# Optimization experiments

Hardware: AMD Instinct MI355X
Metric: run time of the kernel (lower is better)

The kernel has to match this reference:

```python
import jax, jax.numpy as jnp
import numpy as np

N, K, P, C, H, E, Q, G = 50000, 8, 512, 64, 128, 1600000, 500000, 64

def _gelu(x):
    return jax.nn.gelu(x, approximate=False)  # torch F.gelu default = exact erf

def _mlp(x, Wi, bi, Wh, bh, Wo, bo, Wp=None, bp=None):
    # MLP: lin_in -> gelu -> hid -> (proj skip if in>hidden) -> skip+gelu -> lin_out
    skip = x if Wp is None else x @ Wp.T + bp
    h = _gelu(x @ Wi.T + bi)
    h = h @ Wh.T + bh
    return (skip + _gelu(h)) @ Wo.T + bo

def _sage(x, src, dst, Wl, bl, Wr, n):
    # PyG SAGEConv: mean-aggregate source features at dst, then lin_l(agg)+lin_r(x)
    s = jax.ops.segment_sum(x[src], dst, num_segments=n)
    cnt = jax.ops.segment_sum(jnp.ones((src.shape[0], 1), x.dtype), dst, num_segments=n)
    agg = s / jnp.maximum(cnt, 1.0)
    return agg @ Wl.T + bl + x @ Wr.T

def setup_inputs():
    key = jax.random.key(0)
    ks = iter(jax.random.split(key, 64))
    def lin(o, i):
        return (jax.random.normal(next(ks), (o, i), jnp.float32) / np.sqrt(i)).astype(jnp.float32)
    def bias(o):
        return jnp.zeros((o,), jnp.float32)
    inp = {}
    inp["x"] = jax.random.normal(next(ks), (N, K, P), jnp.float32)
    inp["batch"] = jnp.sort(jax.random.randint(next(ks), (N,), 0, G))
    inp["edge_index"] = jax.random.randint(next(ks), (2, E), 0, N)
    inp["src_idx"] = jax.random.randint(next(ks), (Q,), 0, N)
    inp["dst_idx"] = jax.random.randint(next(ks), (Q,), 0, N)
    # Embedder.mlp : MLP(P, P, H) with proj (P > H)
    inp.update(em_in_W=lin(H, P), em_in_b=bias(H), em_hid_W=lin(H, H), em_hid_b=bias(H),
               em_out_W=lin(P, H), em_out_b=bias(P), em_proj_W=lin(H, P), em_proj_b=bias(H))
    # Embedder.rho : MLP(P, C, H) with proj
    inp.update(rho_in_W=lin(H, P), rho_in_b=bias(H), rho_hid_W=lin(H, H), rho_hid_b=bias(H),
               rho_out_W=lin(C, H), rho_out_b=bias(C), rho_proj_W=lin(H, P), rho_proj_b=bias(H))
    for i in (1, 2, 3):
        inp[f"c{i}_ll_W"] = lin(C, C); inp[f"c{i}_ll_b"] = bias(C); inp[f"c{i}_lr_W"] = lin(C, C)
    # head MLP(3C, 2C, 2C) with proj (3C > 2C)
    inp.update(h1_in_W=lin(H, 3 * C), h1_in_b=bias(H), h1_hid_W=lin(H, H), h1_hid_b=bias(H),
               h1_out_W=lin(2 * C, H), h1_out_b=bias(2 * C), h1_proj_W=lin(H, 3 * C), h1_proj_b=bias(H))
    # head MLP(2C, 1, 2C), no proj
    inp.update(h2_in_W=lin(H, 2 * C), h2_in_b=bias(H), h2_hid_W=lin(H, H), h2_hid_b=bias(H),
               h2_out_W=lin(1, H), h2_out_b=bias(1))
    return inp

def reference(x, batch, edge_index, src_idx, dst_idx,
              em_in_W, em_in_b, em_hid_W, em_hid_b, em_out_W, em_out_b, em_proj_W, em_proj_b,
              rho_in_W, rho_in_b, rho_hid_W, rho_hid_b, rho_out_W, rho_out_b, rho_proj_W, rho_proj_b,
              c1_ll_W, c1_ll_b, c1_lr_W, c2_ll_W, c2_ll_b, c2_lr_W, c3_ll_W, c3_ll_b, c3_lr_W,
              h1_in_W, h1_in_b, h1_hid_W, h1_hid_b, h1_out_W, h1_out_b, h1_proj_W, h1_proj_b,
              h2_in_W, h2_in_b, h2_hid_W, h2_hid_b, h2_out_W, h2_out_b):
    n = x.shape[0]
    # Embedder: per-point MLP, gelu, sum over point-set dim, then rho (dropout = eval identity)
    h = _gelu(_mlp(x, em_in_W, em_in_b, em_hid_W, em_hid_b, em_out_W, em_out_b, em_proj_W, em_proj_b))
    z = _mlp(h.sum(-2), rho_in_W, rho_in_b, rho_hid_W, rho_hid_b, rho_out_W, rho_out_b, rho_proj_W, rho_proj_b)
    src, dst = edge_index[0], edge_index[1]
    z = z + _gelu(_sage(z, src, dst, c1_ll_W, c1_ll_b, c1_lr_W, n))
    z = z + _gelu(_sage(z, src, dst, c2_ll_W, c2_ll_b, c2_lr_W, n))
    z = z + _gelu(_sage(z, src, dst, c3_ll_W, c3_ll_b, c3_lr_W, n))
    node_embeddings = z
    # global_max_pool keyed by batch id, broadcast back via gather
    graph_emb = jax.ops.segment_max(z, batch, num_segments=G)
    ge = graph_emb[batch[src_idx]]  # == graph_emb[batch][src_idx]
    se, de = z[src_idx], z[dst_idx]
    xy = jnp.concatenate([se, de, ge], axis=-1)
    yx = jnp.concatenate([de, se, ge], axis=-1)
    def head(q):
        t = jax.nn.relu(_mlp(q, h1_in_W, h1_in_b, h1_hid_W, h1_hid_b, h1_out_W, h1_out_b, h1_proj_W, h1_proj_b))
        return _mlp(t, h2_in_W, h2_in_b, h2_hid_W, h2_hid_b, h2_out_W, h2_out_b)
    return (node_embeddings, (head(xy), head(yx)), xy)
```

## Files before the change

### kernel.cpp

```cpp
#include <hip/hip_runtime.h>

typedef unsigned short US;
typedef unsigned int   UI;
typedef short  short8 __attribute__((ext_vector_type(8)));
typedef US     u16x8  __attribute__((ext_vector_type(8)));
typedef float  f32x4  __attribute__((ext_vector_type(4)));

#define DEVI __device__ __forceinline__

DEVI float bf2f(US u){ UI i = ((UI)u) << 16; float f; __builtin_memcpy(&f, &i, 4); return f; }
DEVI US f2bf(float x){ UI i; __builtin_memcpy(&i, &x, 4); UI r = (i + 0x7FFFu + ((i >> 16) & 1u)) >> 16; return (US)r; }
DEVI float gelu_f(float x){
    float x2 = x * x;
    float u  = x * fmaf(x2, 0.0713548193f, 1.5957691216f);
    float e  = __expf(-u);
    return x / (1.0f + e);
}
DEVI UI encf(float f){ UI u; __builtin_memcpy(&u, &f, 4); return (u & 0x80000000u) ? ~u : (u | 0x80000000u); }
DEVI float decf(UI u){ UI b = (u & 0x80000000u) ? (u ^ 0x80000000u) : ~u; float f; __builtin_memcpy(&f, &b, 4); return f; }
DEVI int swz(int r, int c, int ld){ int i = r * ld + c; return i ^ ((r & 7) << 3); }

DEVI UI pkbf(float a, float b){ UI u; asm("v_cvt_pk_bf16_f32 %0, %1, %2" : "=v"(u) : "v"(a), "v"(b)); return u; }
DEVI void st4(US* T, int row, int col, float v0, float v1, float v2, float v3){
    uint2 p; p.x = pkbf(v0, v1); p.y = pkbf(v2, v3);
    *(uint2*)&T[swz(row, col, 256)] = p;
}
DEVI void ld4(const US* T, int row, int col, float& v0, float& v1, float& v2, float& v3){
    uint2 q = *(const uint2*)&T[swz(row, col, 256)];
    v0 = bf2f((US)(q.x & 0xffff)); v1 = bf2f((US)(q.x >> 16));
    v2 = bf2f((US)(q.y & 0xffff)); v3 = bf2f((US)(q.y >> 16));
}

enum : int { O_EmW1 = 0, O_EmWh = 131072, O_EmWo = 147456, O_RhoW1 = 212992,
             O_RhoWh = 344064, O_RhoWo = 360448, O_Cat1 = 368640, O_Cat2 = 376832,
             O_Cat3 = 385024, O_H1W1 = 393216, O_H1Wh = 442368, O_H1Wo = 458752,
             O_H2W1 = 475136, O_H2Wh = 491520, W_TOTAL = 507904 };

template<int NT, int NKC, int NTHR, bool SWAP = false>
DEVI void stageWD(const US* __restrict__ Wg, int Kw, const US* __restrict__ A, int lda,
                  int ab0, int ab1, int ab2, int arow0, US* Wb, int tid, f32x4 (&acc)[NT])
{
    const int lane = tid & 63;
    const int wc = (tid >> 6) & 1;
    constexpr int SLAB = NT * 32 * 64;
    #pragma unroll
    for (int n = 0; n < NT; ++n) acc[n] = (f32x4){0.f, 0.f, 0.f, 0.f};
    constexpr int J = (NT * 256) / NTHR;
    u16x8 wreg[J];
    #pragma unroll
    for (int j = 0; j < J; ++j) {
        const int c = tid + NTHR * j;
        wreg[j] = *(const u16x8*)(Wg + (size_t)(c >> 3) * Kw + (c & 7) * 8);
    }
    #pragma unroll
    for (int j = 0; j < J; ++j) {
        const int c = tid + NTHR * j;
        *(u16x8*)&Wb[swz(c >> 3, (c & 7) * 8, 64)] = wreg[j];
    }
    #pragma unroll
    for (int kc = 0; kc < NKC; ++kc) {
        __syncthreads();
        if (kc + 1 < NKC) {
            #pragma unroll
            for (int j = 0; j < J; ++j) {
                const int c = tid + NTHR * j;
                wreg[j] = *(const u16x8*)(Wg + (size_t)(c >> 3) * Kw + (kc + 1) * 64 + (c & 7) * 8);
            }
        }
        const int ab = (kc == 0) ? ab0 : ((kc == 1) ? ab1 : ab2);
        const int bufr = (kc & 1) * SLAB;
        #pragma unroll
        for (int sub = 0; sub < 2; ++sub) {
            const int kk = sub * 32 + ((lane >> 4) << 3);
            short8 a = *(const short8*)&A[swz(arow0 + (lane & 15), ab + kk, lda)];
            #pragma unroll
            for (int n = 0; n < NT; ++n) {
                short8 b = *(const short8*)&Wb[bufr + swz(wc * (NT * 16) + n * 16 + (lane & 15), kk, 64)];
                if (SWAP) acc[n] = __builtin_amdgcn_mfma_f32_16x16x32_bf16(b, a, acc[n], 0, 0, 0);
                else      acc[n] = __builtin_amdgcn_mfma_f32_16x16x32_bf16(a, b, acc[n], 0, 0, 0);
            }
        }
        if (kc + 1 < NKC) {
            const int bufw = ((kc + 1) & 1) * SLAB;
            #pragma unroll
            for (int j = 0; j < J; ++j) {
                const int c = tid + NTHR * j;
                *(u16x8*)&Wb[bufw + swz(c >> 3, (c & 7) * 8, 64)] = wreg[j];
            }
        }
    }
    __syncthreads();
}

__global__ __launch_bounds__(1024, 4)
void embed_fused(const float* __restrict__ x, const US* __restrict__ WB,
                 const float* __restrict__ b_in, const float* __restrict__ b_proj,
                 const float* __restrict__ b_hid, const float* __restrict__ b_out,
                 US* __restrict__ Ss)
{
    __shared__ __align__(16) US T1[128 * 256];
    __shared__ __align__(16) US Wb[2 * 16384];
    __shared__ __align__(16) US As[128 * 64];
    const int tid = threadIdx.x, lane = tid & 63, w = tid >> 6;
    const int wr = w >> 1, wc = w & 1;
    const int grow0 = blockIdx.x * 128;
    const int row0 = wr * 16 + ((lane >> 4) << 2);

    {
        f32x4 acc[8];
        #pragma unroll
        for (int n = 0; n < 8; ++n) acc[n] = (f32x4){0.f, 0.f, 0.f, 0.f};
        const float* xr = x + (size_t)(grow0 + (tid >> 3)) * 512 + (tid & 7) * 8;
        float4 a0, a1;
        u16x8 wreg[2];
        auto loadA = [&](int kc) { a0 = *(const float4*)(xr + kc * 64); a1 = *(const float4*)(xr + kc * 64 + 4); };
        auto loadW = [&](int kc) {
            #pragma unroll
            for (int j = 0; j < 2; ++j) {
                const int c = tid + 1024 * j;
                wreg[j] = *(const u16x8*)(WB + O_EmW1 + (size_t)(c >> 3) * 512 + kc * 64 + (c & 7) * 8);
            }
        };
        loadA(0); loadW(0);
        for (int kc = 0; kc < 8; ++kc) {
            __syncthreads();
            {
                u16x8 v;
                v[0] = f2bf(a0.x); v[1] = f2bf(a0.y); v[2] = f2bf(a0.z); v[3] = f2bf(a0.w);
                v[4] = f2bf(a1.x); v[5] = f2bf(a1.y); v[6] = f2bf(a1.z); v[7] = f2bf(a1.w);
                *(u16x8*)&As[swz(tid >> 3, (tid & 7) * 8, 64)] = v;
                #pragma unroll
                for (int j = 0; j < 2; ++j) {
                    const int c = tid + 1024 * j;
                    *(u16x8*)&Wb[swz(c >> 3, (c & 7) * 8, 64)] = wreg[j];
                }
            }
            __syncthreads();
            if (kc < 7) { loadA(kc + 1); loadW(kc + 1); }
            #pragma unroll
            for (int sub = 0; sub < 2; ++sub) {
                const int kk = sub * 32 + ((lane >> 4) << 3);
                short8 a = *(const short8*)&As[swz(wr * 16 + (lane & 15), kk, 64)];
                #pragma unroll
                for (int n = 0; n < 8; ++n) {
                    short8 b = *(const short8*)&Wb[swz(wc * 128 + n * 16 + (lane & 15), kk, 64)];
                    acc[n] = __builtin_amdgcn_mfma_f32_16x16x32_bf16(a, b, acc[n], 0, 0, 0);
                }
            }
        }
        __syncthreads();
        #pragma unroll
        for (int n = 0; n < 8; ++n) {
            const int col = wc * 128 + n * 16 + (lane & 15);
            const float bv = (col < 128) ? b_in[col] : b_proj[col - 128];
            #pragma unroll
            for (int r = 0; r < 4; ++r) {
                float v = acc[n][r] + bv;
                if (col < 128) v = gelu_f(v);
                T1[swz(row0 + r, col, 256)] = f2bf(v);
            }
        }
    }
    {
        f32x4 acc[4];
        stageWD<4, 2, 1024>(WB + O_EmWh, 128, T1, 256, 0, 64, 0, wr * 16, Wb, tid, acc);
        #pragma unroll
        for (int n = 0; n < 4; ++n) {
            const int col = wc * 64 + n * 16 + (lane & 15);
            const float bv = b_hid[col];
            #pragma unroll
            for (int r = 0; r < 4; ++r) {
                const float sv = bf2f(T1[swz(row0 + r, 128 + col, 256)]);
                T1[swz(row0 + r, col, 256)] = f2bf(gelu_f(acc[n][r] + bv) + sv);
            }
        }
    }
    for (int p2 = 0; p2 < 2; ++p2) {
        f32x4 acc[8];
        stageWD<8, 2, 1024>(WB + O_EmWo + (size_t)(p2 * 256) * 128, 128, T1, 256, 0, 64, 0, wr * 16, Wb, tid, acc);
        #pragma unroll
        for (int n = 0; n < 8; ++n) {
            const int col = wc * 128 + n * 16 + (lane & 15);
            const float bv = b_out[p2 * 256 + col];
            float s = 0.f;
            #pragma unroll
            for (int r = 0; r < 4; ++r) s += gelu_f(acc[n][r] + bv);
            s += __shfl_xor(s, 16);
            if (((lane >> 4) & 1) == 0) {
                const int node = (grow0 >> 3) + wr * 2 + (lane >> 5);
                Ss[(size_t)node * 512 + p2 * 256 + col] = f2bf(s);
            }
        }
    }
}

__global__ __launch_bounds__(512, 2)
void rho_fused(const US* __restrict__ Ss, const US* __restrict__ WB,
               const float* __restrict__ b_in, const float* __restrict__ b_proj,
               const float* __restrict__ b_hid, const float* __restrict__ b_out,
               US* __restrict__ zo, int N)
{
    __shared__ __align__(16) US T1[64 * 256];
    __shared__ __align__(16) US Wb[256 * 64];
    __shared__ __align__(16) US As[64 * 64];
    const int tid = threadIdx.x, lane = tid & 63, w = tid >> 6;
    const int wr = w >> 1, wc = w & 1;
    const int grow0 = blockIdx.x * 64;
    const int row0 = wr * 16 + ((lane >> 4) << 2);

    {
        f32x4 acc[8];
        #pragma unroll
        for (int n = 0; n < 8; ++n) acc[n] = (f32x4){0.f, 0.f, 0.f, 0.f};
        int arow = grow0 + (tid >> 3); if (arow >= N) arow = N - 1;
        const US* srow = Ss + (size_t)arow * 512 + (tid & 7) * 8;
        u16x8 areg, wreg[4];
        auto loadA = [&](int kc) { areg = *(const u16x8*)(srow + kc * 64); };
        auto loadW = [&](int kc) {
            #pragma unroll
            for (int j = 0; j < 4; ++j) {
                const int c = tid + 512 * j;
                wreg[j] = *(const u16x8*)(WB + O_RhoW1 + (size_t)(c >> 3) * 512 + kc * 64 + (c & 7) * 8);
            }
        };
        loadA(0); loadW(0);
        for (int kc = 0; kc < 8; ++kc) {
            __syncthreads();
            *(u16x8*)&As[swz(tid >> 3, (tid & 7) * 8, 64)] = areg;
            #pragma unroll
            for (int j = 0; j < 4; ++j) {
                const int c = tid + 512 * j;
                *(u16x8*)&Wb[swz(c >> 3, (c & 7) * 8, 64)] = wreg[j];
            }
            __syncthreads();
            if (kc < 7) { loadA(kc + 1); loadW(kc + 1); }
            #pragma unroll
            for (int sub = 0; sub < 2; ++sub) {
                const int kk = sub * 32 + ((lane >> 4) << 3);
                short8 a = *(const short8*)&As[swz(wr * 16 + (lane & 15), kk, 64)];
                #pragma unroll
                for (int n = 0; n < 8; ++n) {
                    short8 b = *(const short8*)&Wb[swz(wc * 128 + n * 16 + (lane & 15), kk, 64)];
                    acc[n] = __builtin_amdgcn_mfma_f32_16x16x32_bf16(a, b, acc[n], 0, 0, 0);
                }
            }
        }
        __syncthreads();
        #pragma unroll
        for (int n = 0; n < 8; ++n) {
            const int col = wc * 128 + n * 16 + (lane & 15);
            const float bv = (col < 128) ? b_in[col] : b_proj[col - 128];
            #pragma unroll
            for (int r = 0; r < 4; ++r) {
                float v = acc[n][r] + bv;
                if (col < 128) v = gelu_f(v);
                T1[swz(row0 + r, col, 256)] = f2bf(v);
            }
        }
    }
    {
        f32x4 acc[4];
        stageWD<4, 2, 512>(WB + O_RhoWh, 128, T1, 256, 0, 64, 0, wr * 16, Wb, tid, acc);
        #pragma unroll
        for (int n = 0; n < 4; ++n) {
            const int col = wc * 64 + n * 16 + (lane & 15);
            const float bv = b_hid[col];
            #pragma unroll
            for (int r = 0; r < 4; ++r) {
                const float sv = bf2f(T1[swz(row0 + r, 128 + col, 256)]);
                T1[swz(row0 + r, col, 256)] = f2bf(gelu_f(acc[n][r] + bv) + sv);
            }
        }
    }
    {
        f32x4 acc[2];
        stageWD<2, 2, 512>(WB + O_RhoWo, 128, T1, 256, 0, 64, 0, wr * 16, Wb, tid, acc);
        #pragma unroll
        for (int n = 0; n < 2; ++n) {
            const int col = wc * 32 + n * 16 + (lane & 15);
            const float bv = b_out[col];
            #pragma unroll
            for (int r = 0; r < 4; ++r) {
                const int node = grow0 + row0 + r;
                if (node < N) zo[(size_t)node * 64 + col] = f2bf(acc[n][r] + bv);
            }
        }
    }
}

__global__ __launch_bounds__(1024, 4)
void head_fused(const int* __restrict__ srcq, const int* __restrict__ dstq,
                const int* __restrict__ batch, const US* __restrict__ z,
                const US* __restrict__ geb, const US* __restrict__ WB,
                const float* __restrict__ b1_in, const float* __restrict__ b1_proj,
                const float* __restrict__ b1_hid, const float* __restrict__ b1_out,
                const float* __restrict__ b2_in, const float* __restrict__ b2_hid,
                const float* __restrict__ w2_out, const float* __restrict__ b2_out,
                float* __restrict__ outH, float* __restrict__ outXY, int Q)
{
    __shared__ __align__(16) US A0[64 * 192];
    __shared__ __align__(16) US T1[128 * 256];
    __shared__ __align__(16) US Wb[2 * 16384];
    __shared__ float wout_s[128];
    const int tid = threadIdx.x, lane = tid & 63, w = tid >> 6;
    const int wr = w >> 1, wc = w & 1;
    const int q0 = blockIdx.x * 64;
    const int s1a = (wr < 4) ? 0 : 64;
    const int s1b = (wr < 4) ? 64 : 0;
    const int arowS1 = (wr & 3) * 16;
    const int rowS1 = (wr >> 2) * 64 + arowS1 + (lane & 15);
    const int rowT  = wr * 16 + (lane & 15);
    {
        if (tid < 512) {
            const int r = tid >> 3, h = tid & 7;
            const int q = q0 + r;
            const int qc = (q < Q) ? q : (Q - 1);
            const int s = srcq[qc], d = dstq[qc];
            const int g = batch[s];
            *(u16x8*)&A0[swz(r, h * 8, 192)]       = *(const u16x8*)(z + (size_t)s * 64 + h * 8);
            *(u16x8*)&A0[swz(r, 64 + h * 8, 192)]  = *(const u16x8*)(z + (size_t)d * 64 + h * 8);
            *(u16x8*)&A0[swz(r, 128 + h * 8, 192)] = *(const u16x8*)(geb + (size_t)g * 64 + h * 8);
        }
        if (tid < 128) wout_s[tid] = w2_out[tid];
    }
    __syncthreads();
    {
        #pragma unroll
        for (int jj = 0; jj < 3; ++jj) {
            const int f = tid + 1024 * jj;
            const int row = f / 48;
            const int c4 = (f - row * 48) * 4;
            if (q0 + row < Q) {
                const US* p = &A0[swz(row, c4, 192)];
                float4 o;
                o.x = bf2f(p[0]); o.y = bf2f(p[1]); o.z = bf2f(p[2]); o.w = bf2f(p[3]);
                *(float4*)&outXY[(size_t)(q0 + row) * 192 + c4] = o;
            }
        }
    }
    {
        f32x4 acc8[8];
        stageWD<8, 3, 1024, true>(WB + O_H1W1, 192, A0, 192, s1a, s1b, 128, arowS1, Wb, tid, acc8);
        #pragma unroll
        for (int n = 0; n < 8; ++n) {
            const int col = wc * 128 + n * 16 + ((lane >> 4) << 2);
            float4 bv = (col < 128) ? *(const float4*)&b1_in[col]
                                    : *(const float4*)&b1_proj[col - 128];
            float v0 = acc8[n][0] + bv.x, v1 = acc8[n][1] + bv.y;
            float v2 = acc8[n][2] + bv.z, v3 = acc8[n][3] + bv.w;
            if (col < 128) { v0 = gelu_f(v0); v1 = gelu_f(v1); v2 = gelu_f(v2); v3 = gelu_f(v3); }
            st4(T1, rowS1, col, v0, v1, v2, v3);
        }
    }
    f32x4 acc[4];
    stageWD<4, 2, 1024, true>(WB + O_H1Wh, 128, T1, 256, 0, 64, 0, wr * 16, Wb, tid, acc);
    #pragma unroll
    for (int n = 0; n < 4; ++n) {
        const int col = wc * 64 + n * 16 + ((lane >> 4) << 2);
        float4 bv = *(const float4*)&b1_hid[col];
        float s0, s1, s2, s3;
        ld4(T1, rowT, 128 + col, s0, s1, s2, s3);
        st4(T1, rowT, col,
            gelu_f(acc[0 + n][0] * 0.f + acc[n][0] + bv.x) + s0,
            gelu_f(acc[n][1] + bv.y) + s1,
            gelu_f(acc[n][2] + bv.z) + s2,
            gelu_f(acc[n][3] + bv.w) + s3);
    }
    stageWD<4, 2, 1024, true>(WB + O_H1Wo, 128, T1, 256, 0, 64, 0, wr * 16, Wb, tid, acc);
    #pragma unroll
    for (int n = 0; n < 4; ++n) {
        const int col = wc * 64 + n * 16 + ((lane >> 4) << 2);
        float4 bv = *(const float4*)&b1_out[col];
        st4(T1, rowT, 128 + col,
            fmaxf(acc[n][0] + bv.x, 0.f), fmaxf(acc[n][1] + bv.y, 0.f),
            fmaxf(acc[n][2] + bv.z, 0.f), fmaxf(acc[n][3] + bv.w, 0.f));
    }
    stageWD<4, 2, 1024, true>(WB + O_H2W1, 128, T1, 256, 128, 192, 0, wr * 16, Wb, tid, acc);
    #pragma unroll
    for (int n = 0; n < 4; ++n) {
        const int col = wc * 64 + n * 16 + ((lane >> 4) << 2);
        float4 bv = *(const float4*)&b2_in[col];
        st4(T1, rowT, col,
            gelu_f(acc[n][0] + bv.x), gelu_f(acc[n][1] + bv.y),
            gelu_f(acc[n][2] + bv.z), gelu_f(acc[n][3] + bv.w));
    }
    stageWD<4, 2, 1024, true>(WB + O_H2Wh, 128, T1, 256, 0, 64, 0, wr * 16, Wb, tid, acc);
    #pragma unroll
    for (int n = 0; n < 4; ++n) {
        const int col = wc * 64 + n * 16 + ((lane >> 4) << 2);
        float4 bv = *(const float4*)&b2_hid[col];
        float t0, t1, t2, t3;
        ld4(T1, rowT, 128 + col, t0, t1, t2, t3);
        st4(T1, rowT, col,
            gelu_f(acc[n][0] + bv.x) + t0, gelu_f(acc[n][1] + bv.y) + t1,
            gelu_f(acc[n][2] + bv.z) + t2, gelu_f(acc[n][3] + bv.w) + t3);
    }
    __syncthreads();
    {
        const int r = tid >> 3, h = tid & 7;
        float a = 0.f;
        u16x8 v0 = *(const u16x8*)&T1[swz(r, h * 16, 256)];
        u16x8 v1 = *(const u16x8*)&T1[swz(r, h * 16 + 8, 256)];
        #pragma unroll
        for (int e = 0; e < 8; ++e) {
            a += bf2f(v0[e]) * wout_s[h * 16 + e];
            a += bf2f(v1[e]) * wout_s[h * 16 + 8 + e];
        }
        a += __shfl_xor(a, 4);
        a += __shfl_xor(a, 2);
        a += __shfl_xor(a, 1);
        const int q = q0 + (r & 63);
        if ((lane & 7) == 0 && q < Q) outH[(size_t)(r >> 6) * Q + q] = a + b2_out[0];
    }
}

__global__ __launch_bounds__(256, 2)
void sage_gemm(const US* __restrict__ zin, const US* __restrict__ agg,
               const US* __restrict__ Wc, const float* __restrict__ bias,
               US* __restrict__ zout, int N)
{
    __shared__ __align__(16) US As[128 * 128];
    __shared__ __align__(16) US Ws[64 * 128];
    const int tid = threadIdx.x, lane = tid & 63, w = tid >> 6;
    const int grow0 = blockIdx.x * 128;
    {
        const int r = tid >> 1, h = tid & 1;
        int row = grow0 + r; if (row >= N) row = N - 1;
        const US* src = h ? (zin + (size_t)row * 64) : (agg + (size_t)row * 64);
        #pragma unroll
        for (int j = 0; j < 8; ++j)
            *(u16x8*)&As[swz(r, h * 64 + 8 * j, 128)] = *(const u16x8*)(src + 8 * j);
    }
    #pragma unroll
    for (int j = 0; j < 4; ++j) {
        const int c = tid + 256 * j;
        *(u16x8*)&Ws[swz(c >> 4, (c & 15) * 8, 128)] =
            *(const u16x8*)(Wc + (size_t)(c >> 4) * 128 + (c & 15) * 8);
    }
    __syncthreads();
    const int rbw = w * 32;
    f32x4 acc[2][4];
    #pragma unroll
    for (int m = 0; m < 2; ++m)
        #pragma unroll
        for (int n = 0; n < 4; ++n) acc[m][n] = (f32x4){0.f, 0.f, 0.f, 0.f};
    #pragma unroll
    for (int kc = 0; kc < 2; ++kc)
        #pragma unroll
        for (int sub = 0; sub < 2; ++sub) {
            const int kk = kc * 64 + sub * 32 + ((lane >> 4) << 3);
            short8 a[2], b[4];
            #pragma unroll
            for (int m = 0; m < 2; ++m) a[m] = *(const short8*)&As[swz(rbw + m * 16 + (lane & 15), kk, 128)];
            #pragma unroll
            for (int n = 0; n < 4; ++n) b[n] = *(const short8*)&Ws[swz(n * 16 + (lane & 15), kk, 128)];
            #pragma unroll
            for (int m = 0; m < 2; ++m)
                #pragma unroll
                for (int n = 0; n < 4; ++n)
                    acc[m][n] = __builtin_amdgcn_mfma_f32_16x16x32_bf16(a[m], b[n], acc[m][n], 0, 0, 0);
        }
    #pragma unroll
    for (int m = 0; m < 2; ++m) {
        const int row0 = rbw + m * 16 + ((lane >> 4) << 2);
        #pragma unroll
        for (int n = 0; n < 4; ++n) {
            const int col = n * 16 + (lane & 15);
            const float bv = bias[col];
            #pragma unroll
            for (int r = 0; r < 4; ++r) {
                const int node = grow0 + row0 + r;
                if (node < N) {
                    const float v = gelu_f(acc[m][n][r] + bv) + bf2f(zin[(size_t)node * 64 + col]);
                    zout[(size_t)node * 64 + col] = f2bf(v);
                }
            }
        }
    }
}

struct WSeg { const float* src; int dst; int n; int rl; int ldd; };
struct WPrm { WSeg s[20]; };

__global__ void prep_w(WPrm p, US* __restrict__ wb)
{
    WSeg sg = p.s[blockIdx.x];
    for (int i = threadIdx.x; i < sg.n; i += 256) {
        const int idx = sg.dst + (i / sg.rl) * sg.ldd + (i % sg.rl);
        wb[idx] = f2bf(sg.src[i]);
    }
}

__global__ void count_k(const int* __restrict__ dst, int* __restrict__ cnt, int E)
{
    int e = blockIdx.x * 256 + threadIdx.x;
    if (e < E) atomicAdd(&cnt[dst[e]], 1);
}

__global__ void scan_csr(const int* __restrict__ cnt, int n, int* __restrict__ indp, int* __restrict__ curs)
{
    __shared__ int wsum[16];
    __shared__ int carry_s;
    const int tid = threadIdx.x, lane = tid & 63, w = tid >> 6;
    if (tid == 0) carry_s = 0;
    __syncthreads();
    for (int base = 0; base < n; base += 1024) {
        const int i = base + tid;
        const int v = (i < n) ? cnt[i] : 0;
        int s = v;
        #pragma unroll
        for (int o = 1; o < 64; o <<= 1) { int t = __shfl_up(s, o); if (lane >= o) s += t; }
        if (lane == 63) wsum[w] = s;
        __syncthreads();
        if (w == 0 && lane < 16) {
            int ws2 = wsum[lane];
            #pragma unroll
            for (int o = 1; o < 16; o <<= 1) { int t = __shfl_up(ws2, o); if (lane >= o) ws2 += t; }
            wsum[lane] = ws2;
        }
        __syncthreads();
        const int carry = carry_s;
        const int woff  = (w == 0) ? 0 : wsum[w - 1];
        if (i < n) { const int excl = carry + woff + s - v; indp[i] = excl; curs[i] = excl; }
        __syncthreads();
        if (tid == 0) carry_s = carry + wsum[15];
        __syncthreads();
    }
    if (threadIdx.x == 0) indp[n] = carry_s;
}

__global__ void fill_k(const int* __restrict__ src, const int* __restrict__ dst,
                       int* __restrict__ curs, int* __restrict__ esrc, int E)
{
    int e = blockIdx.x * 256 + threadIdx.x;
    if (e < E) { int p = atomicAdd(&curs[dst[e]], 1); esrc[p] = src[e]; }
}

__global__ void sage_agg(const US* __restrict__ z, const int* __restrict__ indp,
                         const int* __restrict__ esrc, US* __restrict__ agg, int n)
{
    const int w = blockIdx.x * 4 + (threadIdx.x >> 6);
    const int lane = threadIdx.x & 63;
    if (w >= n) return;
    const int beg = indp[w], end = indp[w + 1];
    float acc = 0.f;
    int j = beg;
    for (; j + 4 <= end; j += 4) {
        const int s0 = esrc[j], s1 = esrc[j + 1], s2 = esrc[j + 2], s3 = esrc[j + 3];
        const float v0 = bf2f(z[(size_t)s0 * 64 + lane]);
        const float v1 = bf2f(z[(size_t)s1 * 64 + lane]);
        const float v2 = bf2f(z[(size_t)s2 * 64 + lane]);
        const float v3 = bf2f(z[(size_t)s3 * 64 + lane]);
        acc += (v0 + v1) + (v2 + v3);
    }
    for (; j < end; ++j) acc += bf2f(z[(size_t)esrc[j] * 64 + lane]);
    const float d = (float)(end - beg);
    agg[(size_t)w * 64 + lane] = f2bf(acc / fmaxf(d, 1.0f));
}

__global__ void segmax_k(const US* __restrict__ z, const int* __restrict__ batch,
                         UI* __restrict__ enc, int n, int per)
{
    const int w = blockIdx.x * 4 + (threadIdx.x >> 6);
    const int lane = threadIdx.x & 63;
    const int start = w * per;
    if (start >= n) return;
    const int end = (start + per < n) ? start + per : n;
    int g = batch[start];
    float m = -3.0e38f;
    for (int i = start; i < end; ++i) {
        const int b = batch[i];
        if (b != g) { atomicMax(&enc[(size_t)g * 64 + lane], encf(m)); g = b; m = -3.0e38f; }
        m = fmaxf(m, bf2f(z[(size_t)i * 64 + lane]));
    }
    atomicMax(&enc[(size_t)g * 64 + lane], encf(m));
}

__global__ void decode_ge(const UI* __restrict__ enc, US* __restrict__ geb)
{
    const int i = blockIdx.x * 256 + threadIdx.x;
    if (i < 4096) geb[i] = f2bf(decf(enc[i]));
}

__global__ void copy_bf2f(const US* __restrict__ z, float* __restrict__ o, long n)
{
    long i = (long)blockIdx.x * blockDim.x + threadIdx.x;
    const long stride = (long)gridDim.x * blockDim.x;
    for (; i < n; i += stride) o[i] = bf2f(z[i]);
}

extern "C" void kernel_launch(void* const* d_in, const int* in_sizes, int n_in,
                              void* d_out, int out_size, void* d_ws, size_t ws_size,
                              hipStream_t stream)
{
    (void)in_sizes; (void)n_in; (void)out_size; (void)ws_size;

    const float* x      = (const float*)d_in[0];
    const int*   batch  = (const int*)d_in[1];
    const int*   eidx   = (const int*)d_in[2];
    const int*   srcq   = (const int*)d_in[3];
    const int*   dstq   = (const int*)d_in[4];
    const float* em_in_b   = (const float*)d_in[6];
    const float* em_hid_b  = (const float*)d_in[8];
    const float* em_out_b  = (const float*)d_in[10];
    const float* em_proj_b = (const float*)d_in[12];
    const float* rho_in_b  = (const float*)d_in[14];
    const float* rho_hid_b = (const float*)d_in[16];
    const float* rho_out_b = (const float*)d_in[18];
    const float* rho_proj_b= (const float*)d_in[20];
    const float* c_ll_W[3] = {(const float*)d_in[21], (const float*)d_in[24], (const float*)d_in[27]};
    const float* c_ll_b[3] = {(const float*)d_in[22], (const float*)d_in[25], (const float*)d_in[28]};
    const float* c_lr_W[3] = {(const float*)d_in[23], (const float*)d_in[26], (const float*)d_in[29]};
    const float* h1_in_b   = (const float*)d_in[31];
    const float* h1_hid_b  = (const float*)d_in[33];
    const float* h1_out_b  = (const float*)d_in[35];
    const float* h1_proj_b = (const float*)d_in[37];
    const float* h2_in_b   = (const float*)d_in[39];
    const float* h2_hid_b  = (const float*)d_in[41];
    const float* h2_out_W  = (const float*)d_in[42];
    const float* h2_out_b  = (const float*)d_in[43];

    const int N = 50000, E = 1600000, Q = 500000;
    float* out = (float*)d_out;

    char* wsb = (char*)d_ws;
    size_t off = 0;
    auto ALLOC = [&](size_t bytes) -> char* {
        char* p = wsb + off; off = (off + bytes + 255) & ~(size_t)255; return p;
    };
    US*  WB   = (US*)ALLOC((size_t)W_TOTAL * 2);
    US*  Ss   = (US*)ALLOC((size_t)N * 512 * 2);
    US*  z0   = (US*)ALLOC((size_t)N * 64 * 2);
    US*  z1   = (US*)ALLOC((size_t)N * 64 * 2);
    US*  aggB = (US*)ALLOC((size_t)N * 64 * 2);
    int* cnt  = (int*)ALLOC((size_t)N * 4);
    int* indp = (int*)ALLOC((size_t)(N + 1) * 4);
    int* curs = (int*)ALLOC((size_t)N * 4);
    int* esrc = (int*)ALLOC((size_t)E * 4);
    UI*  enc  = (UI*)ALLOC(4096 * 4);
    US*  geb  = (US*)ALLOC(4096 * 2);

    const int catOff[3] = {O_Cat1, O_Cat2, O_Cat3};

    WPrm pw; int si = 0;
    auto SEG = [&](const float* s, int o, int n, int rl, int ldd) {
        pw.s[si].src = s; pw.s[si].dst = o; pw.s[si].n = n; pw.s[si].rl = rl; pw.s[si].ldd = ldd; ++si;
    };
    SEG((const float*)d_in[5],  O_EmW1,          65536, 65536, 65536);
    SEG((const float*)d_in[11], O_EmW1 + 65536,  65536, 65536, 65536);
    SEG((const float*)d_in[7],  O_EmWh,          16384, 16384, 16384);
    SEG((const float*)d_in[9],  O_EmWo,          65536, 65536, 65536);
    SEG((const float*)d_in[13], O_RhoW1,         65536, 65536, 65536);
    SEG((const float*)d_in[19], O_RhoW1 + 65536, 65536, 65536, 65536);
    SEG((const float*)d_in[15], O_RhoWh,         16384, 16384, 16384);
    SEG((const float*)d_in[17], O_RhoWo,          8192,  8192,  8192);
    for (int i = 0; i < 3; ++i) {
        SEG(c_ll_W[i], catOff[i],      4096, 64, 128);
        SEG(c_lr_W[i], catOff[i] + 64, 4096, 64, 128);
    }
    SEG((const float*)d_in[30], O_H1W1,          24576, 24576, 24576);
    SEG((const float*)d_in[36], O_H1W1 + 24576,  24576, 24576, 24576);
    SEG((const float*)d_in[32], O_H1Wh,          16384, 16384, 16384);
    SEG((const float*)d_in[34], O_H1Wo,          16384, 16384, 16384);
    SEG((const float*)d_in[38], O_H2W1,          16384, 16384, 16384);
    SEG((const float*)d_in[40], O_H2Wh,          16384, 16384, 16384);
    prep_w<<<dim3(20), dim3(256), 0, stream>>>(pw, WB);

    hipMemsetAsync(cnt, 0, (size_t)N * 4, stream);
    count_k<<<dim3((E + 255) / 256), dim3(256), 0, stream>>>(eidx + E, cnt, E);
    scan_csr<<<dim3(1), dim3(1024), 0, stream>>>(cnt, N, indp, curs);
    fill_k<<<dim3((E + 255) / 256), dim3(256), 0, stream>>>(eidx, eidx + E, curs, esrc, E);

    embed_fused<<<dim3(3125), dim3(1024), 0, stream>>>(x, WB, em_in_b, em_proj_b, em_hid_b, em_out_b, Ss);
    rho_fused<<<dim3((N + 63) / 64), dim3(512), 0, stream>>>(Ss, WB, rho_in_b, rho_proj_b, rho_hid_b, rho_out_b, z0, N);

    US* zin = z0; US* zout = z1;
    for (int ci = 0; ci < 3; ++ci) {
        sage_agg<<<dim3((N + 3) / 4), dim3(256), 0, stream>>>(zin, indp, esrc, aggB, N);
        sage_gemm<<<dim3((N + 127) / 128), dim3(256), 0, stream>>>(zin, aggB, WB + catOff[ci], c_ll_b[ci], zout, N);
        US* t = zin; zin = zout; zout = t;
    }
    US* zf = zin;

    hipMemsetAsync(enc, 0, 4096 * 4, stream);
    segmax_k<<<dim3((N + 511) / 512), dim3(256), 0, stream>>>(zf, batch, enc, N, 128);
    decode_ge<<<dim3(16), dim3(256), 0, stream>>>(enc, geb);

    copy_bf2f<<<dim3(2048), dim3(256), 0, stream>>>(zf, out, (long)N * 64);

    head_fused<<<dim3((Q + 63) / 64), dim3(1024), 0, stream>>>(
        srcq, dstq, batch, zf, geb, WB,
        h1_in_b, h1_proj_b, h1_hid_b, h1_out_b, h2_in_b, h2_hid_b, h2_out_W, h2_out_b,
        out + (size_t)N * 64, out + (size_t)N * 64 + 2 * (size_t)Q, Q);
}
```

Measured before the change: 1.816 ms.

## Feed MFMA A operand from registers and double-buffer weights in embed/rho

The first GEMM stage of embed_fused and rho_fused now loads activation rows straight from global memory into registers in MFMA operand layout, removing the As LDS staging buffer. It swaps the MFMA operand order so the output is transposed, and the epilogues use vectorized st4/ld4 writes. embed_fused also double-buffers the weight tile in LDS, dropping one barrier per k-chunk. The head kernel's output-copy indexing is simplified as well. This cuts LDS traffic and barriers, but adds register pressure and uncoalesced-looking global reads per lane.

```diff
diff --git a/kernel.cpp b/kernel.cpp
--- a/kernel.cpp
+++ b/kernel.cpp
@@ -100,20 +100,25 @@
 {
     __shared__ __align__(16) US T1[128 * 256];
     __shared__ __align__(16) US Wb[2 * 16384];
-    __shared__ __align__(16) US As[128 * 64];
     const int tid = threadIdx.x, lane = tid & 63, w = tid >> 6;
     const int wr = w >> 1, wc = w & 1;
+    const int h = lane >> 4;
     const int grow0 = blockIdx.x * 128;
-    const int row0 = wr * 16 + ((lane >> 4) << 2);
+    const int rowT = wr * 16 + (lane & 15);
 
     {
         f32x4 acc[8];
         #pragma unroll
         for (int n = 0; n < 8; ++n) acc[n] = (f32x4){0.f, 0.f, 0.f, 0.f};
-        const float* xr = x + (size_t)(grow0 + (tid >> 3)) * 512 + (tid & 7) * 8;
-        float4 a0, a1;
+        const float* xp = x + (size_t)(grow0 + rowT) * 512 + h * 8;
+        float4 p00, p01, p10, p11;
         u16x8 wreg[2];
-        auto loadA = [&](int kc) { a0 = *(const float4*)(xr + kc * 64); a1 = *(const float4*)(xr + kc * 64 + 4); };
+        auto loadA = [&](int kc) {
+            p00 = *(const float4*)(xp + kc * 64);
+            p01 = *(const float4*)(xp + kc * 64 + 4);
+            p10 = *(const float4*)(xp + kc * 64 + 32);
+            p11 = *(const float4*)(xp + kc * 64 + 36);
+        };
         auto loadW = [&](int kc) {
             #pragma unroll
             for (int j = 0; j < 2; ++j) {
@@ -121,58 +126,63 @@
                 wreg[j] = *(const u16x8*)(WB + O_EmW1 + (size_t)(c >> 3) * 512 + kc * 64 + (c & 7) * 8);
             }
         };
-        loadA(0); loadW(0);
+        auto writeW = [&](int buf) {
+            #pragma unroll
+            for (int j = 0; j < 2; ++j) {
+                const int c = tid + 1024 * j;
+                *(u16x8*)&Wb[buf * 16384 + swz(c >> 3, (c & 7) * 8, 64)] = wreg[j];
+            }
+        };
+        loadA(0); loadW(0); writeW(0);
         for (int kc = 0; kc < 8; ++kc) {
             __syncthreads();
+            short8 a0, a1;
             {
-                u16x8 v;
-                v[0] = f2bf(a0.x); v[1] = f2bf(a0.y); v[2] = f2bf(a0.z); v[3] = f2bf(a0.w);
-                v[4] = f2bf(a1.x); v[5] = f2bf(a1.y); v[6] = f2bf(a1.z); v[7] = f2bf(a1.w);
-                *(u16x8*)&As[swz(tid >> 3, (tid & 7) * 8, 64)] = v;
-                #pragma unroll
-                for (int j = 0; j < 2; ++j) {
-                    const int c = tid + 1024 * j;
-                    *(u16x8*)&Wb[swz(c >> 3, (c & 7) * 8, 64)] = wreg[j];
-                }
-            }
-            __syncthreads();
+                uint4 q;
+                q.x = pkbf(p00.x, p00.y); q.y = pkbf(p00.z, p00.w);
+                q.z = pkbf(p01.x, p01.y); q.w = pkbf(p01.z, p01.w);
+                __builtin_memcpy(&a0, &q, 16);
+                q.x = pkbf(p10.x, p10.y); q.y = pkbf(p10.z, p10.w);
+                q.z = pkbf(p11.x, p11.y); q.w = pkbf(p11.z, p11.w);
+                __builtin_memcpy(&a1, &q, 16);
+            }
             if (kc < 7) { loadA(kc + 1); loadW(kc + 1); }
-            #pragma unroll
-            for (int sub = 0; sub < 2; ++sub) {
-                const int kk = sub * 32 + ((lane >> 4) << 3);
-                short8 a = *(const short8*)&As[swz(wr * 16 + (lane & 15), kk, 64)];
-                #pragma unroll
-                for (int n = 0; n < 8; ++n) {
-                    short8 b = *(const short8*)&Wb[swz(wc * 128 + n * 16 + (lane & 15), kk, 64)];
-                    acc[n] = __builtin_amdgcn_mfma_f32_16x16x32_bf16(a, b, acc[n], 0, 0, 0);
-                }
-            }
-        }
-        __syncthreads();
+            const int bufr = (kc & 1) * 16384;
+            #pragma unroll
+            for (int n = 0; n < 8; ++n) {
+                short8 b = *(const short8*)&Wb[bufr + swz(wc * 128 + n * 16 + (lane & 15), h * 8, 64)];
+                acc[n] = __builtin_amdgcn_mfma_f32_16x16x32_bf16(b, a0, acc[n], 0, 0, 0);
+            }
+            #pragma unroll
+            for (int n = 0; n < 8; ++n) {
+                short8 b = *(const short8*)&Wb[bufr + swz(wc * 128 + n * 16 + (lane & 15), 32 + h * 8, 64)];
+                acc[n] = __builtin_amdgcn_mfma_f32_16x16x32_bf16(b, a1, acc[n], 0, 0, 0);
+            }
+            if (kc < 7) writeW((kc + 1) & 1);
+        }
         #pragma unroll
         for (int n = 0; n < 8; ++n) {
-            const int col = wc * 128 + n * 16 + (lane & 15);
-            const float bv = (col < 128) ? b_in[col] : b_proj[col - 128];
-            #pragma unroll
-            for (int r = 0; r < 4; ++r) {
-                float v = acc[n][r] + bv;
-                if (col < 128) v = gelu_f(v);
-                T1[swz(row0 + r, col, 256)] = f2bf(v);
-            }
+            const int col = wc * 128 + n * 16 + h * 4;
+            float4 bv = (col < 128) ? *(const float4*)&b_in[col]
+                                    : *(const float4*)&b_proj[col - 128];
+            float v0 = acc[n][0] + bv.x, v1 = acc[n][1] + bv.y;
+            float v2 = acc[n][2] + bv.z, v3 = acc[n][3] + bv.w;
+            if (col < 128) { v0 = gelu_f(v0); v1 = gelu_f(v1); v2 = gelu_f(v2); v3 = gelu_f(v3); }
+            st4(T1, rowT, col, v0, v1, v2, v3);
         }
     }
     {
         f32x4 acc[4];
-        stageWD<4, 2, 1024>(WB + O_EmWh, 128, T1, 256, 0, 64, 0, wr * 16, Wb, tid, acc);
+        stageWD<4, 2, 1024, true>(WB + O_EmWh, 128, T1, 256, 0, 64, 0, wr * 16, Wb, tid, acc);
         #pragma unroll
         for (int n = 0; n < 4; ++n) {
-            const int col = wc * 64 + n * 16 + (lane & 15);
-            const float bv = b_hid[col];
-            #pragma unroll
-            for (int r = 0; r < 4; ++r) {
-                const float sv = bf2f(T1[swz(row0 + r, 128 + col, 256)]);
-                T1[swz(row0 + r, col, 256)] = f2bf(gelu_f(acc[n][r] + bv) + sv);
-            }
+            const int col = wc * 64 + n * 16 + h * 4;
+            float4 bv = *(const float4*)&b_hid[col];
+            float s0, s1, s2, s3;
+            ld4(T1, rowT, 128 + col, s0, s1, s2, s3);
+            st4(T1, rowT, col,
+                gelu_f(acc[n][0] + bv.x) + s0, gelu_f(acc[n][1] + bv.y) + s1,
+                gelu_f(acc[n][2] + bv.z) + s2, gelu_f(acc[n][3] + bv.w) + s3);
         }
     }
     for (int p2 = 0; p2 < 2; ++p2) {
@@ -202,20 +212,23 @@
 {
     __shared__ __align__(16) US T1[64 * 256];
     __shared__ __align__(16) US Wb[256 * 64];
-    __shared__ __align__(16) US As[64 * 64];
     const int tid = threadIdx.x, lane = tid & 63, w = tid >> 6;
     const int wr = w >> 1, wc = w & 1;
+    const int h = lane >> 4;
     const int grow0 = blockIdx.x * 64;
-    const int row0 = wr * 16 + ((lane >> 4) << 2);
+    const int rowT = wr * 16 + (lane & 15);
 
     {
         f32x4 acc[8];
         #pragma unroll
         for (int n = 0; n < 8; ++n) acc[n] = (f32x4){0.f, 0.f, 0.f, 0.f};
-        int arow = grow0 + (tid >> 3); if (arow >= N) arow = N - 1;
-        const US* srow = Ss + (size_t)arow * 512 + (tid & 7) * 8;
-        u16x8 areg, wreg[4];
-        auto loadA = [&](int kc) { areg = *(const u16x8*)(srow + kc * 64); };
+        int arow = grow0 + rowT; if (arow >= N) arow = N - 1;
+        const US* sp = Ss + (size_t)arow * 512 + h * 8;
+        u16x8 a0r, a1r, wreg[4];
+        auto loadA = [&](int kc) {
+            a0r = *(const u16x8*)(sp + kc * 64);
+            a1r = *(const u16x8*)(sp + kc * 64 + 32);
+        };
         auto loadW = [&](int kc) {
             #pragma unroll
             for (int j = 0; j < 4; ++j) {
@@ -226,50 +239,52 @@
         loadA(0); loadW(0);
         for (int kc = 0; kc < 8; ++kc) {
             __syncthreads();
-            *(u16x8*)&As[swz(tid >> 3, (tid & 7) * 8, 64)] = areg;
             #pragma unroll
             for (int j = 0; j < 4; ++j) {
                 const int c = tid + 512 * j;
                 *(u16x8*)&Wb[swz(c >> 3, (c & 7) * 8, 64)] = wreg[j];
             }
             __syncthreads();
-            if (kc < 7) { loadA(kc + 1); loadW(kc + 1); }
-            #pragma unroll
-            for (int sub = 0; sub < 2; ++sub) {
-                const int kk = sub * 32 + ((lane >> 4) << 3);
-                short8 a = *(const short8*)&As[swz(wr * 16 + (lane & 15), kk, 64)];
-                #pragma unroll
-                for (int n = 0; n < 8; ++n) {
-                    short8 b = *(const short8*)&Wb[swz(wc * 128 + n * 16 + (lane & 15), kk, 64)];
-                    acc[n] = __builtin_amdgcn_mfma_f32_16x16x32_bf16(a, b, acc[n], 0, 0, 0);
-                }
-            }
+            if (kc < 7) loadW(kc + 1);
+            short8 a0, a1;
+            __builtin_memcpy(&a0, &a0r, 16);
+            __builtin_memcpy(&a1, &a1r, 16);
+            #pragma unroll
+            for (int n = 0; n < 8; ++n) {
+                short8 b = *(const short8*)&Wb[swz(wc * 128 + n * 16 + (lane & 15), h * 8, 64)];
+                acc[n] = __builtin_amdgcn_mfma_f32_16x16x32_bf16(b, a0, acc[n], 0, 0, 0);
+            }
+            #pragma unroll
+            for (int n = 0; n < 8; ++n) {
+                short8 b = *(const short8*)&Wb[swz(wc * 128 + n * 16 + (lane & 15), 32 + h * 8, 64)];
+                acc[n] = __builtin_amdgcn_mfma_f32_16x16x32_bf16(b, a1, acc[n], 0, 0, 0);
+            }
+            if (kc < 7) loadA(kc + 1);
         }
         __syncthreads();
         #pragma unroll
         for (int n = 0; n < 8; ++n) {
-            const int col = wc * 128 + n * 16 + (lane & 15);
-            const float bv = (col < 128) ? b_in[col] : b_proj[col - 128];
-            #pragma unroll
-            for (int r = 0; r < 4; ++r) {
-                float v = acc[n][r] + bv;
-                if (col < 128) v = gelu_f(v);
-                T1[swz(row0 + r, col, 256)] = f2bf(v);
-            }
+            const int col = wc * 128 + n * 16 + h * 4;
+            float4 bv = (col < 128) ? *(const float4*)&b_in[col]
+                                    : *(const float4*)&b_proj[col - 128];
+            float v0 = acc[n][0] + bv.x, v1 = acc[n][1] + bv.y;
+            float v2 = acc[n][2] + bv.z, v3 = acc[n][3] + bv.w;
+            if (col < 128) { v0 = gelu_f(v0); v1 = gelu_f(v1); v2 = gelu_f(v2); v3 = gelu_f(v3); }
+            st4(T1, rowT, col, v0, v1, v2, v3);
         }
     }
     {
         f32x4 acc[4];
-        stageWD<4, 2, 512>(WB + O_RhoWh, 128, T1, 256, 0, 64, 0, wr * 16, Wb, tid, acc);
+        stageWD<4, 2, 512, true>(WB + O_RhoWh, 128, T1, 256, 0, 64, 0, wr * 16, Wb, tid, acc);
         #pragma unroll
         for (int n = 0; n < 4; ++n) {
-            const int col = wc * 64 + n * 16 + (lane & 15);
-            const float bv = b_hid[col];
-            #pragma unroll
-            for (int r = 0; r < 4; ++r) {
-                const float sv = bf2f(T1[swz(row0 + r, 128 + col, 256)]);
-                T1[swz(row0 + r, col, 256)] = f2bf(gelu_f(acc[n][r] + bv) + sv);
-            }
+            const int col = wc * 64 + n * 16 + h * 4;
+            float4 bv = *(const float4*)&b_hid[col];
+            float s0, s1, s2, s3;
+            ld4(T1, rowT, 128 + col, s0, s1, s2, s3);
+            st4(T1, rowT, col,
+                gelu_f(acc[n][0] + bv.x) + s0, gelu_f(acc[n][1] + bv.y) + s1,
+                gelu_f(acc[n][2] + bv.z) + s2, gelu_f(acc[n][3] + bv.w) + s3);
         }
     }
     {
@@ -281,7 +296,7 @@
             const float bv = b_out[col];
             #pragma unroll
             for (int r = 0; r < 4; ++r) {
-                const int node = grow0 + row0 + r;
+                const int node = grow0 + wr * 16 + h * 4 + r;
                 if (node < N) zo[(size_t)node * 64 + col] = f2bf(acc[n][r] + bv);
             }
         }
@@ -312,24 +327,24 @@
     const int rowT  = wr * 16 + (lane & 15);
     {
         if (tid < 512) {
-            const int r = tid >> 3, h = tid & 7;
+            const int r = tid >> 3, hh = tid & 7;
             const int q = q0 + r;
             const int qc = (q < Q) ? q : (Q - 1);
             const int s = srcq[qc], d = dstq[qc];
             const int g = batch[s];
-            *(u16x8*)&A0[swz(r, h * 8, 192)]       = *(const u16x8*)(z + (size_t)s * 64 + h * 8);
-            *(u16x8*)&A0[swz(r, 64 + h * 8, 192)]  = *(const u16x8*)(z + (size_t)d * 64 + h * 8);
-            *(u16x8*)&A0[swz(r, 128 + h * 8, 192)] = *(const u16x8*)(geb + (size_t)g * 64 + h * 8);
+            *(u16x8*)&A0[swz(r, hh * 8, 192)]       = *(const u16x8*)(z + (size_t)s * 64 + hh * 8);
+            *(u16x8*)&A0[swz(r, 64 + hh * 8, 192)]  = *(const u16x8*)(z + (size_t)d * 64 + hh * 8);
+            *(u16x8*)&A0[swz(r, 128 + hh * 8, 192)] = *(const u16x8*)(geb + (size_t)g * 64 + hh * 8);
         }
         if (tid < 128) wout_s[tid] = w2_out[tid];
     }
     __syncthreads();
     {
+        const int row = tid >> 4;
+        const int qu  = tid & 15;
         #pragma unroll
         for (int jj = 0; jj < 3; ++jj) {
-            const int f = tid + 1024 * jj;
-            const int row = f / 48;
-            const int c4 = (f - row * 48) * 4;
+            const int c4 = (jj * 16 + qu) * 4;
             if (q0 + row < Q) {
                 const US* p = &A0[swz(row, c4, 192)];
                 float4 o;
@@ -361,10 +376,8 @@
         float s0, s1, s2, s3;
         ld4(T1, rowT, 128 + col, s0, s1, s2, s3);
         st4(T1, rowT, col,
-            gelu_f(acc[0 + n][0] * 0.f + acc[n][0] + bv.x) + s0,
-            gelu_f(acc[n][1] + bv.y) + s1,
-            gelu_f(acc[n][2] + bv.z) + s2,
-            gelu_f(acc[n][3] + bv.w) + s3);
+            gelu_f(acc[n][0] + bv.x) + s0, gelu_f(acc[n][1] + bv.y) + s1,
+            gelu_f(acc[n][2] + bv.z) + s2, gelu_f(acc[n][3] + bv.w) + s3);
     }
     stageWD<4, 2, 1024, true>(WB + O_H1Wo, 128, T1, 256, 0, 64, 0, wr * 16, Wb, tid, acc);
     #pragma unroll
@@ -397,14 +410,14 @@
     }
     __syncthreads();
     {
-        const int r = tid >> 3, h = tid & 7;
+        const int r = tid >> 3, hh = tid & 7;
         float a = 0.f;
-        u16x8 v0 = *(const u16x8*)&T1[swz(r, h * 16, 256)];
-        u16x8 v1 = *(const u16x8*)&T1[swz(r, h * 16 + 8, 256)];
+        u16x8 v0 = *(const u16x8*)&T1[swz(r, hh * 16, 256)];
+        u16x8 v1 = *(const u16x8*)&T1[swz(r, hh * 16 + 8, 256)];
         #pragma unroll
         for (int e = 0; e < 8; ++e) {
-            a += bf2f(v0[e]) * wout_s[h * 16 + e];
-            a += bf2f(v1[e]) * wout_s[h * 16 + 8 + e];
+            a += bf2f(v0[e]) * wout_s[hh * 16 + e];
+            a += bf2f(v1[e]) * wout_s[hh * 16 + 8 + e];
         }
         a += __shfl_xor(a, 4);
         a += __shfl_xor(a, 2);
@@ -424,12 +437,12 @@
     const int tid = threadIdx.x, lane = tid & 63, w = tid >> 6;
     const int grow0 = blockIdx.x * 128;
     {
-        const int r = tid >> 1, h = tid & 1;
+        const int r = tid >> 1, hh = tid & 1;
         int row = grow0 + r; if (row >= N) row = N - 1;
-        const US* src = h ? (zin + (size_t)row * 64) : (agg + (size_t)row * 64);
+        const US* src = hh ? (zin + (size_t)row * 64) : (agg + (size_t)row * 64);
         #pragma unroll
         for (int j = 0; j < 8; ++j)
-            *(u16x8*)&As[swz(r, h * 64 + 8 * j, 128)] = *(const u16x8*)(src + 8 * j);
+            *(u16x8*)&As[swz(r, hh * 64 + 8 * j, 128)] = *(const u16x8*)(src + 8 * j);
     }
     #pragma unroll
     for (int j = 0; j < 4; ++j) {
```

New measurement: 1.836 ms. Within noise of the previous version (+1.1%).
